# Kernel optimization log

Hardware: AMD Instinct MI355X
Metric: run time of the kernel (lower is better)

Reference implementation:

```python
import jax, jax.numpy as jnp
import numpy as np

B, C, H, W = 8, 256, 128, 128
K = 3  # conv kernel size, padding=1 -> SAME


def conv3x3(x, w, b):
    # x: [B,C,H,W], w: [O,I,K,K], b: [O]
    y = jax.lax.conv_general_dilated(
        x, w, window_strides=(1, 1), padding='SAME',
        dimension_numbers=('NCHW', 'OIHW', 'NCHW'))
    return y + b[None, :, None, None]


def setup_inputs() -> dict:
    key = jax.random.key(0)
    ks = jax.random.split(key, 7)
    fan_in = C * K * K
    s = 1.0 / np.sqrt(fan_in)
    x = jax.random.normal(ks[0], (B, C, H, W), dtype=jnp.float32)
    Wq = jax.random.uniform(ks[1], (C, C, K, K), jnp.float32, -s, s)
    bq = jax.random.uniform(ks[2], (C,), jnp.float32, -s, s)
    Wk = jax.random.uniform(ks[3], (C, C, K, K), jnp.float32, -s, s)
    bk = jax.random.uniform(ks[4], (C,), jnp.float32, -s, s)
    Wv = jax.random.uniform(ks[5], (C, C, K, K), jnp.float32, -s, s)
    bv = jax.random.uniform(ks[6], (C,), jnp.float32, -s, s)
    return {'x': x, 'Wq': Wq, 'bq': bq, 'Wk': Wk, 'bk': bk, 'Wv': Wv, 'bv': bv}


def reference(x, Wq, bq, Wk, bk, Wv, bv):
    b_, c_, h_, w_ = x.shape
    residual = x
    q = jax.nn.relu(conv3x3(x, Wq, bq))  # [B,C,H,W]
    k = jax.nn.relu(conv3x3(x, Wk, bk))  # [B,C,H,W]
    v = conv3x3(x, Wv, bv)               # [B,C,H,W]
    # per-(batch,channel) spatial matmul: [H,W] @ [H,W] -> [H,W] (requires H==W)
    attn = jnp.einsum('bcij,bcjk->bcik', q, k)
    # softmax over the flattened H*W positions jointly per (b,c)
    attn = jax.nn.softmax(attn.reshape(b_, c_, h_ * w_), axis=-1).reshape(b_, c_, h_, w_)
    y = jnp.einsum('bcij,bcjk->bcik', attn, v)
    return y + residual
```

## Files before the change

### kernel.cpp

```cpp
#include <hip/hip_runtime.h>

#define BB 8
#define CC 256
#define HH 128
#define WW 128
#define HW (HH*WW)

typedef float f32x4 __attribute__((ext_vector_type(4)));
typedef short s16x8 __attribute__((ext_vector_type(8)));

__device__ inline unsigned short f2bf(float f) {
  union { float f; unsigned int u; } un;
  un.f = f;
  unsigned int u = un.u;
  return (unsigned short)((u + 0x7fffu + ((u >> 16) & 1u)) >> 16);
}

__global__ __launch_bounds__(256) void k_prepass(const float* __restrict__ x,
                                                 unsigned short* __restrict__ xbf) {
  __shared__ float tile[64][68];
  int bh = blockIdx.x;
  int b = bh >> 7, h = bh & 127;
  int w0 = blockIdx.y * 64;
  int c0 = blockIdx.z * 64;
  int t = threadIdx.x;
  {
    int c = t >> 2, wq = (t & 3) << 4;
    const float4* src = reinterpret_cast<const float4*>(
        x + (((size_t)(b * CC + c0 + c) * HH + h) * WW + w0 + wq));
    float4 v0 = src[0], v1 = src[1], v2 = src[2], v3 = src[3];
    *reinterpret_cast<float4*>(&tile[c][wq + 0])  = v0;
    *reinterpret_cast<float4*>(&tile[c][wq + 4])  = v1;
    *reinterpret_cast<float4*>(&tile[c][wq + 8])  = v2;
    *reinterpret_cast<float4*>(&tile[c][wq + 12]) = v3;
  }
  __syncthreads();
  {
    int w = t >> 2, cg = (t & 3) << 4;
    unsigned short tmp[16];
#pragma unroll
    for (int i = 0; i < 16; ++i) tmp[i] = f2bf(tile[cg + i][w]);
    unsigned short* dst = xbf + ((size_t)(b * HH + h) * WW + w0 + w) * CC + c0 + cg;
    *reinterpret_cast<int4*>(dst)     = *reinterpret_cast<int4*>(tmp);
    *reinterpret_cast<int4*>(dst + 8) = *reinterpret_cast<int4*>(tmp + 8);
  }
}

__global__ __launch_bounds__(256) void k_repack(const float* __restrict__ Wq,
                                                const float* __restrict__ Wk,
                                                const float* __restrict__ Wv,
                                                unsigned short* __restrict__ Wp) {
  int idx = blockIdx.x * 256 + threadIdx.x;
  if (idx >= 8 * 9 * 768 * 32) return;
  int ci = idx & 31;
  int tmp = idx >> 5;
  int focs = tmp % 768;
  int tmp2 = tmp / 768;
  int tap = tmp2 % 9;
  int chunk = tmp2 / 9;
  int cv = focs >> 8, oc = focs & 255;
  int cin = chunk * 32 + ci;
  const float* Wsrc = (cv == 0) ? Wq : ((cv == 1) ? Wk : Wv);
  Wp[idx] = f2bf(Wsrc[(size_t)(oc * 256 + cin) * 9 + tap]);
}

#define PADC 40
__global__ __launch_bounds__(256, 2) void k_conv(const unsigned short* __restrict__ xbf,
                                                 const unsigned short* __restrict__ Wp,
                                                 const float* __restrict__ bq,
                                                 const float* __restrict__ bk,
                                                 const float* __restrict__ bv,
                                                 unsigned short* __restrict__ qkv) {
  __shared__ unsigned short xs[4][132][PADC];
  __shared__ float bias_s[128];
  int bid = blockIdx.x;
  int v_ = (bid & 7) * 384 + (bid >> 3);
  int mtile = v_ % 6;
  int bhp = v_ / 6;
  int b = bhp >> 6;
  int h0 = (bhp & 63) * 2;
  int t = threadIdx.x;
  if (t < 128) {
    int focs = mtile * 128 + t;
    int cv = focs >> 8, oc = focs & 255;
    const float* bp = (cv == 0) ? bq : ((cv == 1) ? bk : bv);
    bias_s[t] = bp[oc];
  }
  int lane = t & 63, wave = t >> 6;
  int wm = wave >> 1, wn = wave & 1;
  int l15 = lane & 15, lg = lane >> 4;
  f32x4 acc[4][8] = {};
  for (int chunk = 0; chunk < 8; ++chunk) {
    __syncthreads();
    for (int g = t; g < 2080; g += 256) {
      int oct = g & 3;
      int wc = (g >> 2) % 130;
      int r = (g >> 2) / 130;
      int hin = h0 + r - 1, win = wc - 1;
      int4 val = {0, 0, 0, 0};
      if ((unsigned)hin < 128u && (unsigned)win < 128u) {
        val = *reinterpret_cast<const int4*>(
            xbf + ((size_t)(b * HH + hin) * WW + win) * CC + chunk * 32 + oct * 8);
      }
      *reinterpret_cast<int4*>(&xs[r][wc][oct * 8]) = val;
    }
    __syncthreads();
    const unsigned short* wpc = Wp + (size_t)chunk * (9 * 768 * 32)
                                + (size_t)(mtile * 128 + wm * 64 + l15) * 32 + lg * 8;
#pragma unroll
    for (int tap = 0; tap < 9; ++tap) {
      const int r = tap / 3, s = tap % 3;
      s16x8 afr[4], bfr[8];
      const unsigned short* ap = wpc + tap * (768 * 32);
#pragma unroll
      for (int m = 0; m < 4; ++m)
        afr[m] = *reinterpret_cast<const s16x8*>(ap + m * (16 * 32));
#pragma unroll
      for (int n = 0; n < 8; ++n)
        bfr[n] = *reinterpret_cast<const s16x8*>(&xs[wn + r][n * 16 + l15 + s][lg * 8]);
#pragma unroll
      for (int m = 0; m < 4; ++m)
#pragma unroll
        for (int n = 0; n < 8; ++n)
          acc[m][n] = __builtin_amdgcn_mfma_f32_16x16x32_bf16(afr[m], bfr[n], acc[m][n], 0, 0, 0);
    }
  }
#pragma unroll
  for (int m = 0; m < 4; ++m) {
#pragma unroll
    for (int n = 0; n < 8; ++n) {
      int wcol = n * 16 + l15;
      int h = h0 + wn;
#pragma unroll
      for (int rg = 0; rg < 4; ++rg) {
        int rl = wm * 64 + m * 16 + lg * 4 + rg;
        float vv = acc[m][n][rg] + bias_s[rl];
        int focs = mtile * 128 + rl;
        if (focs < 512) vv = fmaxf(vv, 0.0f);
        int cv = focs >> 8, oc = focs & 255;
        qkv[(size_t)(cv * 2048 + b * 256 + oc) * HW + h * WW + wcol] = f2bf(vv);
      }
    }
  }
}

#define PADA 136
__global__ __launch_bounds__(256) void k_attn(const unsigned short* __restrict__ qkv,
                                              const float* __restrict__ x,
                                              float* __restrict__ out) {
  __shared__ unsigned short al[128][PADA];
  __shared__ unsigned short kt[128][PADA];
  __shared__ unsigned short vt[128][PADA];
  __shared__ float red[8];
  int bc = blockIdx.x;
  const unsigned short* qp = qkv + (size_t)bc * HW;
  const unsigned short* kp = qkv + (size_t)(2048 + bc) * HW;
  const unsigned short* vp = qkv + (size_t)(4096 + bc) * HW;
  int t = threadIdx.x;
  for (int g = t; g < HW; g += 256) {
    int row = g >> 7, col = g & 127;
    kt[col][row] = kp[g];
    vt[col][row] = vp[g];
  }
  __syncthreads();
  int lane = t & 63, wave = t >> 6;
  int wm = wave >> 1, wn = wave & 1;
  int l15 = lane & 15, lg = lane >> 4;
  f32x4 acc[4][4] = {};
#pragma unroll
  for (int kk = 0; kk < 4; ++kk) {
    s16x8 af[4], bfr[4];
#pragma unroll
    for (int m = 0; m < 4; ++m)
      af[m] = *reinterpret_cast<const s16x8*>(qp + (size_t)(wm * 64 + m * 16 + l15) * WW + kk * 32 + lg * 8);
#pragma unroll
    for (int n = 0; n < 4; ++n)
      bfr[n] = *reinterpret_cast<const s16x8*>(&kt[wn * 64 + n * 16 + l15][kk * 32 + lg * 8]);
#pragma unroll
    for (int m = 0; m < 4; ++m)
#pragma unroll
      for (int n = 0; n < 4; ++n)
        acc[m][n] = __builtin_amdgcn_mfma_f32_16x16x32_bf16(af[m], bfr[n], acc[m][n], 0, 0, 0);
  }
  float lm = -3.0e38f;
#pragma unroll
  for (int m = 0; m < 4; ++m)
#pragma unroll
    for (int n = 0; n < 4; ++n)
#pragma unroll
      for (int rg = 0; rg < 4; ++rg)
        lm = fmaxf(lm, acc[m][n][rg]);
  for (int off = 32; off > 0; off >>= 1) lm = fmaxf(lm, __shfl_xor(lm, off));
  if (lane == 0) red[wave] = lm;
  __syncthreads();
  float M = fmaxf(fmaxf(red[0], red[1]), fmaxf(red[2], red[3]));
  float ls = 0.0f;
#pragma unroll
  for (int m = 0; m < 4; ++m)
#pragma unroll
    for (int n = 0; n < 4; ++n)
#pragma unroll
      for (int rg = 0; rg < 4; ++rg)
        ls += __expf(acc[m][n][rg] - M);
  for (int off = 32; off > 0; off >>= 1) ls += __shfl_xor(ls, off);
  if (lane == 0) red[4 + wave] = ls;
  __syncthreads();
  float inv = 1.0f / (red[4] + red[5] + red[6] + red[7]);
#pragma unroll
  for (int m = 0; m < 4; ++m) {
#pragma unroll
    for (int n = 0; n < 4; ++n) {
      int col = wn * 64 + n * 16 + l15;
#pragma unroll
      for (int rg = 0; rg < 4; ++rg) {
        int row = wm * 64 + m * 16 + lg * 4 + rg;
        al[row][col] = f2bf(__expf(acc[m][n][rg] - M) * inv);
      }
    }
  }
  __syncthreads();
  f32x4 o_[4][4] = {};
#pragma unroll
  for (int kk = 0; kk < 4; ++kk) {
    s16x8 af[4], bfr[4];
#pragma unroll
    for (int m = 0; m < 4; ++m)
      af[m] = *reinterpret_cast<const s16x8*>(&al[wm * 64 + m * 16 + l15][kk * 32 + lg * 8]);
#pragma unroll
    for (int n = 0; n < 4; ++n)
      bfr[n] = *reinterpret_cast<const s16x8*>(&vt[wn * 64 + n * 16 + l15][kk * 32 + lg * 8]);
#pragma unroll
    for (int m = 0; m < 4; ++m)
#pragma unroll
      for (int n = 0; n < 4; ++n)
        o_[m][n] = __builtin_amdgcn_mfma_f32_16x16x32_bf16(af[m], bfr[n], o_[m][n], 0, 0, 0);
  }
  const float* xp = x + (size_t)bc * HW;
  float* op = out + (size_t)bc * HW;
#pragma unroll
  for (int m = 0; m < 4; ++m) {
#pragma unroll
    for (int n = 0; n < 4; ++n) {
      int col = wn * 64 + n * 16 + l15;
#pragma unroll
      for (int rg = 0; rg < 4; ++rg) {
        int row = wm * 64 + m * 16 + lg * 4 + rg;
        op[row * WW + col] = o_[m][n][rg] + xp[row * WW + col];
      }
    }
  }
}

extern "C" void kernel_launch(void* const* d_in, const int* in_sizes, int n_in,
                              void* d_out, int out_size, void* d_ws, size_t ws_size,
                              hipStream_t stream) {
  const float* x  = (const float*)d_in[0];
  const float* Wq = (const float*)d_in[1];
  const float* bq = (const float*)d_in[2];
  const float* Wk = (const float*)d_in[3];
  const float* bk = (const float*)d_in[4];
  const float* Wv = (const float*)d_in[5];
  const float* bv = (const float*)d_in[6];
  float* out = (float*)d_out;

  unsigned short* xbf = (unsigned short*)d_ws;
  unsigned short* qkv = xbf + (size_t)33554432;
  unsigned short* Wp  = qkv + (size_t)3 * 33554432;

  dim3 g0(1024, 2, 4);
  k_prepass<<<g0, 256, 0, stream>>>(x, xbf);
  k_repack<<<6912, 256, 0, stream>>>(Wq, Wk, Wv, Wp);
  k_conv<<<3072, 256, 0, stream>>>(xbf, Wp, bq, bk, bv, qkv);
  k_attn<<<2048, 256, 0, stream>>>(qkv, x, out);
}
```

Measured before the change: 583.2 us.

## Double-buffer conv input via async global-to-LDS loads with 32x32 MFMA tiles

The conv kernel now stages each 32-channel input chunk into a double-buffered LDS tile using global_load_lds direct copies, prefetching the next chunk while computing the current one. The padding layout is replaced by an XOR swizzle, and out-of-bounds rows read from a zeroed workspace buffer. Compute switches from 16x16x32 to 32x32x16 bf16 MFMA, reusing each loaded input row across the three vertical taps. The aim is to hide load latency, cut barriers and LDS traffic, at the cost of more LDS per block and more complex indexing.

```diff
diff --git a/kernel.cpp b/kernel.cpp
--- a/kernel.cpp
+++ b/kernel.cpp
@@ -7,6 +7,7 @@
 #define HW (HH*WW)
 
 typedef float f32x4 __attribute__((ext_vector_type(4)));
+typedef float f32x16 __attribute__((ext_vector_type(16)));
 typedef short s16x8 __attribute__((ext_vector_type(8)));
 
 __device__ inline unsigned short f2bf(float f) {
@@ -14,6 +15,12 @@
   un.f = f;
   unsigned int u = un.u;
   return (unsigned short)((u + 0x7fffu + ((u >> 16) & 1u)) >> 16);
+}
+
+__device__ __forceinline__ void gload_lds16(const void* g, void* l) {
+  __builtin_amdgcn_global_load_lds(
+      (const __attribute__((address_space(1))) unsigned int*)g,
+      (__attribute__((address_space(3))) unsigned int*)l, 16, 0, 0);
 }
 
 __global__ __launch_bounds__(256) void k_prepass(const float* __restrict__ x,
@@ -49,7 +56,12 @@
 __global__ __launch_bounds__(256) void k_repack(const float* __restrict__ Wq,
                                                 const float* __restrict__ Wk,
                                                 const float* __restrict__ Wv,
-                                                unsigned short* __restrict__ Wp) {
+                                                unsigned short* __restrict__ Wp,
+                                                unsigned short* __restrict__ zp) {
+  if (blockIdx.x == 0 && threadIdx.x < 64) {
+    int4 z = {0, 0, 0, 0};
+    reinterpret_cast<int4*>(zp)[threadIdx.x] = z;
+  }
   int idx = blockIdx.x * 256 + threadIdx.x;
   if (idx >= 8 * 9 * 768 * 32) return;
   int ci = idx & 31;
@@ -64,14 +76,14 @@
   Wp[idx] = f2bf(Wsrc[(size_t)(oc * 256 + cin) * 9 + tap]);
 }
 
-#define PADC 40
 __global__ __launch_bounds__(256, 2) void k_conv(const unsigned short* __restrict__ xbf,
                                                  const unsigned short* __restrict__ Wp,
+                                                 const unsigned short* __restrict__ zp,
                                                  const float* __restrict__ bq,
                                                  const float* __restrict__ bk,
                                                  const float* __restrict__ bv,
                                                  unsigned short* __restrict__ qkv) {
-  __shared__ unsigned short xs[4][132][PADC];
+  __shared__ unsigned short xs[2][4][132][32];
   __shared__ float bias_s[128];
   int bid = blockIdx.x;
   int v_ = (bid & 7) * 384 + (bid >> 3);
@@ -80,65 +92,110 @@
   int b = bhp >> 6;
   int h0 = (bhp & 63) * 2;
   int t = threadIdx.x;
+  int lane = t & 63, wave = t >> 6;
+  int wm = wave >> 1, wq = wave & 1;
+  int l31 = lane & 31, lg1 = lane >> 5;
+
   if (t < 128) {
     int focs = mtile * 128 + t;
     int cv = focs >> 8, oc = focs & 255;
     const float* bp = (cv == 0) ? bq : ((cv == 1) ? bk : bv);
     bias_s[t] = bp[oc];
   }
-  int lane = t & 63, wave = t >> 6;
-  int wm = wave >> 1, wn = wave & 1;
-  int l15 = lane & 15, lg = lane >> 4;
-  f32x4 acc[4][8] = {};
+  {
+    int cell = t >> 4;
+    int bf_ = cell >> 3, r_ = (cell >> 1) & 3;
+    int wc_ = (cell & 1) ? 129 : 0;
+    *reinterpret_cast<int*>(reinterpret_cast<char*>(&xs[bf_][r_][wc_][0]) + (t & 15) * 4) = 0;
+  }
+
+  int l2 = lane >> 2, l4 = lane & 3;
+  int osw = l4 ^ (((l2 + 1) >> 1) & 3);
+  int rsta = wave;
+  int hin = h0 + rsta - 1;
+  bool inb = ((unsigned)hin < 128u);
+  const unsigned short* srow =
+      xbf + ((size_t)(b * HH + (inb ? hin : 0)) * WW + l2) * CC + osw * 8;
+  const unsigned short* zsrc = zp + lane * 8;
+
+  auto STAGE = [&](int bufn, int chunk) {
+    char* d0 = reinterpret_cast<char*>(&xs[bufn][rsta][1][0]);
+    if (inb) {
+      const unsigned short* s0 = srow + chunk * 32;
+#pragma unroll
+      for (int j = 0; j < 8; ++j)
+        gload_lds16(s0 + j * (16 * CC), d0 + j * 1024);
+    } else {
+#pragma unroll
+      for (int j = 0; j < 8; ++j)
+        gload_lds16(zsrc, d0 + j * 1024);
+    }
+  };
+
+  f32x16 acc[2][2][2] = {};
+  STAGE(0, 0);
+  __syncthreads();
+  int buf = 0;
   for (int chunk = 0; chunk < 8; ++chunk) {
-    __syncthreads();
-    for (int g = t; g < 2080; g += 256) {
-      int oct = g & 3;
-      int wc = (g >> 2) % 130;
-      int r = (g >> 2) / 130;
-      int hin = h0 + r - 1, win = wc - 1;
-      int4 val = {0, 0, 0, 0};
-      if ((unsigned)hin < 128u && (unsigned)win < 128u) {
-        val = *reinterpret_cast<const int4*>(
-            xbf + ((size_t)(b * HH + hin) * WW + win) * CC + chunk * 32 + oct * 8);
+    if (chunk < 7) STAGE(buf ^ 1, chunk + 1);
+    const unsigned short (*xsb)[132][32] = xs[buf];
+    const unsigned short* ap0 = Wp + (size_t)chunk * (9 * 768 * 32)
+        + (size_t)(mtile * 128 + wm * 64 + l31) * 32 + lg1 * 8;
+#pragma unroll
+    for (int ss = 0; ss < 3; ++ss) {
+#pragma unroll
+      for (int kk = 0; kk < 2; ++kk) {
+        s16x8 Bf[4][2];
+#pragma unroll
+        for (int rin = 0; rin < 4; ++rin)
+#pragma unroll
+        for (int nt = 0; nt < 2; ++nt) {
+          int wc = wq * 64 + nt * 32 + l31 + ss;
+          int pslot = (kk * 2 + lg1) ^ ((wc >> 1) & 3);
+          Bf[rin][nt] = *reinterpret_cast<const s16x8*>(
+              reinterpret_cast<const char*>(&xsb[rin][0][0]) + wc * 64 + pslot * 16);
+        }
+        s16x8 Af[3][2];
+#pragma unroll
+        for (int rr = 0; rr < 3; ++rr)
+#pragma unroll
+        for (int mt = 0; mt < 2; ++mt)
+          Af[rr][mt] = *reinterpret_cast<const s16x8*>(
+              ap0 + (rr * 3 + ss) * (768 * 32) + mt * 1024 + kk * 16);
+#pragma unroll
+        for (int rr = 0; rr < 3; ++rr)
+#pragma unroll
+        for (int row = 0; row < 2; ++row)
+#pragma unroll
+        for (int mt = 0; mt < 2; ++mt)
+#pragma unroll
+        for (int nt = 0; nt < 2; ++nt)
+          acc[mt][row][nt] = __builtin_amdgcn_mfma_f32_32x32x16_bf16(
+              Af[rr][mt], Bf[row + rr][nt], acc[mt][row][nt], 0, 0, 0);
       }
-      *reinterpret_cast<int4*>(&xs[r][wc][oct * 8]) = val;
-    }
-    __syncthreads();
-    const unsigned short* wpc = Wp + (size_t)chunk * (9 * 768 * 32)
-                                + (size_t)(mtile * 128 + wm * 64 + l15) * 32 + lg * 8;
-#pragma unroll
-    for (int tap = 0; tap < 9; ++tap) {
-      const int r = tap / 3, s = tap % 3;
-      s16x8 afr[4], bfr[8];
-      const unsigned short* ap = wpc + tap * (768 * 32);
-#pragma unroll
-      for (int m = 0; m < 4; ++m)
-        afr[m] = *reinterpret_cast<const s16x8*>(ap + m * (16 * 32));
-#pragma unroll
-      for (int n = 0; n < 8; ++n)
-        bfr[n] = *reinterpret_cast<const s16x8*>(&xs[wn + r][n * 16 + l15 + s][lg * 8]);
-#pragma unroll
-      for (int m = 0; m < 4; ++m)
-#pragma unroll
-        for (int n = 0; n < 8; ++n)
-          acc[m][n] = __builtin_amdgcn_mfma_f32_16x16x32_bf16(afr[m], bfr[n], acc[m][n], 0, 0, 0);
-    }
-  }
-#pragma unroll
-  for (int m = 0; m < 4; ++m) {
-#pragma unroll
-    for (int n = 0; n < 8; ++n) {
-      int wcol = n * 16 + l15;
-      int h = h0 + wn;
-#pragma unroll
-      for (int rg = 0; rg < 4; ++rg) {
-        int rl = wm * 64 + m * 16 + lg * 4 + rg;
-        float vv = acc[m][n][rg] + bias_s[rl];
-        int focs = mtile * 128 + rl;
-        if (focs < 512) vv = fmaxf(vv, 0.0f);
-        int cv = focs >> 8, oc = focs & 255;
-        qkv[(size_t)(cv * 2048 + b * 256 + oc) * HW + h * WW + wcol] = f2bf(vv);
+    }
+    if (chunk < 7) __syncthreads();
+    buf ^= 1;
+  }
+
+#pragma unroll
+  for (int mt = 0; mt < 2; ++mt) {
+#pragma unroll
+    for (int row = 0; row < 2; ++row) {
+#pragma unroll
+      for (int nt = 0; nt < 2; ++nt) {
+        int wcol = wq * 64 + nt * 32 + l31;
+        int h = h0 + row;
+#pragma unroll
+        for (int reg = 0; reg < 16; ++reg) {
+          int rloc = (reg & 3) + 8 * (reg >> 2) + 4 * lg1;
+          int floc = wm * 64 + mt * 32 + rloc;
+          float vv = acc[mt][row][nt][reg] + bias_s[floc];
+          int focs = mtile * 128 + floc;
+          if (focs < 512) vv = fmaxf(vv, 0.0f);
+          int cv = focs >> 8, oc = focs & 255;
+          qkv[(size_t)(cv * 2048 + b * 256 + oc) * HW + h * WW + wcol] = f2bf(vv);
+        }
       }
     }
   }
@@ -266,10 +323,11 @@
   unsigned short* xbf = (unsigned short*)d_ws;
   unsigned short* qkv = xbf + (size_t)33554432;
   unsigned short* Wp  = qkv + (size_t)3 * 33554432;
+  unsigned short* zp  = Wp + (size_t)(8 * 9 * 768 * 32);
 
   dim3 g0(1024, 2, 4);
   k_prepass<<<g0, 256, 0, stream>>>(x, xbf);
-  k_repack<<<6912, 256, 0, stream>>>(Wq, Wk, Wv, Wp);
-  k_conv<<<3072, 256, 0, stream>>>(xbf, Wp, bq, bk, bv, qkv);
+  k_repack<<<6912, 256, 0, stream>>>(Wq, Wk, Wv, Wp, zp);
+  k_conv<<<3072, 256, 0, stream>>>(xbf, Wp, zp, bq, bk, bv, qkv);
   k_attn<<<2048, 256, 0, stream>>>(qkv, x, out);
 }
```

New measurement: 575.5 us. About the same (-1.3%).

## Rewrite conv to read padded channel-plane input directly with 32x32 MFMA

Applied to the files above, without the earlier changes.

The prepass now writes input as bf16 planes of 8 channels with zero-padded width columns, plus a zeroed row buffer for out-of-range rows. The conv kernel drops its LDS staging and barriers and loads B fragments straight from global memory via row pointers. It switches to 32x32x16 MFMA with smaller 64-output tiles, twice the blocks, and occupancy 3, and adds setprio around the MFMA bursts. This trades LDS reuse for redundant global/L2 reads of input rows.

```diff
diff --git a/kernel.cpp b/kernel.cpp
--- a/kernel.cpp
+++ b/kernel.cpp
@@ -6,7 +6,10 @@
 #define WW 128
 #define HW (HH*WW)
 
+#define PLANE_B (128 * 130 * 16)
+
 typedef float f32x4 __attribute__((ext_vector_type(4)));
+typedef float f32x16 __attribute__((ext_vector_type(16)));
 typedef short s16x8 __attribute__((ext_vector_type(8)));
 
 __device__ inline unsigned short f2bf(float f) {
@@ -17,7 +20,7 @@
 }
 
 __global__ __launch_bounds__(256) void k_prepass(const float* __restrict__ x,
-                                                 unsigned short* __restrict__ xbf) {
+                                                 char* __restrict__ xb2) {
   __shared__ float tile[64][68];
   int bh = blockIdx.x;
   int b = bh >> 7, h = bh & 127;
@@ -35,14 +38,23 @@
     *reinterpret_cast<float4*>(&tile[c][wq + 12]) = v3;
   }
   __syncthreads();
-  {
-    int w = t >> 2, cg = (t & 3) << 4;
-    unsigned short tmp[16];
-#pragma unroll
-    for (int i = 0; i < 16; ++i) tmp[i] = f2bf(tile[cg + i][w]);
-    unsigned short* dst = xbf + ((size_t)(b * HH + h) * WW + w0 + w) * CC + c0 + cg;
-    *reinterpret_cast<int4*>(dst)     = *reinterpret_cast<int4*>(tmp);
-    *reinterpret_cast<int4*>(dst + 8) = *reinterpret_cast<int4*>(tmp + 8);
+  int w = t & 63, cgi = t >> 6;
+#pragma unroll
+  for (int j2 = 0; j2 < 2; ++j2) {
+    int cgl = cgi * 2 + j2;
+    unsigned short tmp[8];
+#pragma unroll
+    for (int i = 0; i < 8; ++i) tmp[i] = f2bf(tile[cgl * 8 + i][w]);
+    size_t off = (size_t)(b * 32 + blockIdx.z * 8 + cgl) * PLANE_B
+               + ((size_t)h * 130 + (w0 + w + 1)) * 16;
+    *reinterpret_cast<int4*>(xb2 + off) = *reinterpret_cast<int4*>(tmp);
+  }
+  if (t < 8) {
+    int4 z = {0, 0, 0, 0};
+    int wp = (blockIdx.y == 0) ? 0 : 129;
+    size_t off = (size_t)(b * 32 + blockIdx.z * 8 + t) * PLANE_B
+               + ((size_t)h * 130 + wp) * 16;
+    *reinterpret_cast<int4*>(xb2 + off) = z;
   }
 }
 
@@ -64,78 +76,93 @@
   Wp[idx] = f2bf(Wsrc[(size_t)(oc * 256 + cin) * 9 + tap]);
 }
 
-#define PADC 40
-__global__ __launch_bounds__(256, 2) void k_conv(const unsigned short* __restrict__ xbf,
+__global__ __launch_bounds__(256, 3) void k_conv(const char* __restrict__ xb2,
                                                  const unsigned short* __restrict__ Wp,
                                                  const float* __restrict__ bq,
                                                  const float* __restrict__ bk,
                                                  const float* __restrict__ bv,
                                                  unsigned short* __restrict__ qkv) {
-  __shared__ unsigned short xs[4][132][PADC];
-  __shared__ float bias_s[128];
+  __shared__ float bias_s[64];
   int bid = blockIdx.x;
-  int v_ = (bid & 7) * 384 + (bid >> 3);
-  int mtile = v_ % 6;
-  int bhp = v_ / 6;
+  int v_ = (bid & 7) * 768 + (bid >> 3);
+  int mtile = v_ % 12;
+  int bhp = v_ / 12;
   int b = bhp >> 6;
   int h0 = (bhp & 63) * 2;
   int t = threadIdx.x;
-  if (t < 128) {
-    int focs = mtile * 128 + t;
+  int lane = t & 63, wave = t >> 6;
+  int wm = wave >> 1, wq = wave & 1;
+  int l31 = lane & 31, lg1 = lane >> 5;
+
+  if (t < 64) {
+    int focs = mtile * 64 + t;
     int cv = focs >> 8, oc = focs & 255;
     const float* bp = (cv == 0) ? bq : ((cv == 1) ? bk : bv);
     bias_s[t] = bp[oc];
   }
-  int lane = t & 63, wave = t >> 6;
-  int wm = wave >> 1, wn = wave & 1;
-  int l15 = lane & 15, lg = lane >> 4;
-  f32x4 acc[4][8] = {};
+  __syncthreads();
+
+  const char* zbase = xb2 + (size_t)256 * PLANE_B;
+  int woff[2];
+#pragma unroll
+  for (int nt = 0; nt < 2; ++nt)
+    woff[nt] = (lg1 * (128 * 130) + (wq * 64 + nt * 32 + l31)) * 16;
+
+  const size_t CH_STRIDE = (size_t)9 * 768 * 32;
+  const unsigned short* apbase = Wp + (size_t)(mtile * 64 + wm * 32 + l31) * 32 + lg1 * 8;
+
+  f32x16 acc[2][2] = {};
+
   for (int chunk = 0; chunk < 8; ++chunk) {
-    __syncthreads();
-    for (int g = t; g < 2080; g += 256) {
-      int oct = g & 3;
-      int wc = (g >> 2) % 130;
-      int r = (g >> 2) / 130;
-      int hin = h0 + r - 1, win = wc - 1;
-      int4 val = {0, 0, 0, 0};
-      if ((unsigned)hin < 128u && (unsigned)win < 128u) {
-        val = *reinterpret_cast<const int4*>(
-            xbf + ((size_t)(b * HH + hin) * WW + win) * CC + chunk * 32 + oct * 8);
-      }
-      *reinterpret_cast<int4*>(&xs[r][wc][oct * 8]) = val;
+    const unsigned short* ap = apbase + chunk * CH_STRIDE;
+#pragma unroll
+    for (int kk = 0; kk < 2; ++kk) {
+      const char* rowb[4];
+#pragma unroll
+      for (int rin = 0; rin < 4; ++rin) {
+        int hin = h0 + rin - 1;
+        rowb[rin] = ((unsigned)hin < 128u)
+            ? xb2 + (size_t)(b * 32 + chunk * 4 + kk * 2) * PLANE_B + (size_t)hin * (130 * 16)
+            : zbase;
+      }
+#pragma unroll
+      for (int ss = 0; ss < 3; ++ss) {
+        s16x8 Bf[4][2];
+#pragma unroll
+        for (int rin = 0; rin < 4; ++rin)
+#pragma unroll
+        for (int nt = 0; nt < 2; ++nt)
+          Bf[rin][nt] = *reinterpret_cast<const s16x8*>(rowb[rin] + woff[nt] + ss * 16);
+        s16x8 Af[3];
+#pragma unroll
+        for (int rr = 0; rr < 3; ++rr)
+          Af[rr] = *reinterpret_cast<const s16x8*>(ap + (rr * 3 + ss) * (768 * 32) + kk * 16);
+        __builtin_amdgcn_s_setprio(1);
+#pragma unroll
+        for (int rr = 0; rr < 3; ++rr)
+#pragma unroll
+        for (int row = 0; row < 2; ++row)
+#pragma unroll
+        for (int nt = 0; nt < 2; ++nt)
+          acc[row][nt] = __builtin_amdgcn_mfma_f32_32x32x16_bf16(
+              Af[rr], Bf[row + rr][nt], acc[row][nt], 0, 0, 0);
+        __builtin_amdgcn_s_setprio(0);
+      }
     }
-    __syncthreads();
-    const unsigned short* wpc = Wp + (size_t)chunk * (9 * 768 * 32)
-                                + (size_t)(mtile * 128 + wm * 64 + l15) * 32 + lg * 8;
-#pragma unroll
-    for (int tap = 0; tap < 9; ++tap) {
-      const int r = tap / 3, s = tap % 3;
-      s16x8 afr[4], bfr[8];
-      const unsigned short* ap = wpc + tap * (768 * 32);
-#pragma unroll
-      for (int m = 0; m < 4; ++m)
-        afr[m] = *reinterpret_cast<const s16x8*>(ap + m * (16 * 32));
-#pragma unroll
-      for (int n = 0; n < 8; ++n)
-        bfr[n] = *reinterpret_cast<const s16x8*>(&xs[wn + r][n * 16 + l15 + s][lg * 8]);
-#pragma unroll
-      for (int m = 0; m < 4; ++m)
-#pragma unroll
-        for (int n = 0; n < 8; ++n)
-          acc[m][n] = __builtin_amdgcn_mfma_f32_16x16x32_bf16(afr[m], bfr[n], acc[m][n], 0, 0, 0);
-    }
-  }
-#pragma unroll
-  for (int m = 0; m < 4; ++m) {
-#pragma unroll
-    for (int n = 0; n < 8; ++n) {
-      int wcol = n * 16 + l15;
-      int h = h0 + wn;
-#pragma unroll
-      for (int rg = 0; rg < 4; ++rg) {
-        int rl = wm * 64 + m * 16 + lg * 4 + rg;
-        float vv = acc[m][n][rg] + bias_s[rl];
-        int focs = mtile * 128 + rl;
+  }
+
+#pragma unroll
+  for (int row = 0; row < 2; ++row) {
+#pragma unroll
+    for (int nt = 0; nt < 2; ++nt) {
+      int wcol = wq * 64 + nt * 32 + l31;
+      int h = h0 + row;
+#pragma unroll
+      for (int reg = 0; reg < 16; ++reg) {
+        int rloc = (reg & 3) + 8 * (reg >> 2) + 4 * lg1;
+        int floc = wm * 32 + rloc;
+        float vv = acc[row][nt][reg] + bias_s[floc];
+        int focs = mtile * 64 + floc;
         if (focs < 512) vv = fmaxf(vv, 0.0f);
         int cv = focs >> 8, oc = focs & 255;
         qkv[(size_t)(cv * 2048 + b * 256 + oc) * HW + h * WW + wcol] = f2bf(vv);
@@ -263,13 +290,16 @@
   const float* bv = (const float*)d_in[6];
   float* out = (float*)d_out;
 
-  unsigned short* xbf = (unsigned short*)d_ws;
-  unsigned short* qkv = xbf + (size_t)33554432;
-  unsigned short* Wp  = qkv + (size_t)3 * 33554432;
-
+  char* xb2 = (char*)d_ws;
+  size_t zoff = (size_t)256 * PLANE_B;
+  unsigned short* qkv = (unsigned short*)(xb2 + zoff + 270336);
+  unsigned short* Wp  = qkv + (size_t)3 * BB * 256 * HW / 6 * 6;
+  Wp = qkv + (size_t)100663296;
+
+  hipMemsetAsync(xb2 + zoff, 0, 270336, stream);
   dim3 g0(1024, 2, 4);
-  k_prepass<<<g0, 256, 0, stream>>>(x, xbf);
+  k_prepass<<<g0, 256, 0, stream>>>(x, xb2);
   k_repack<<<6912, 256, 0, stream>>>(Wq, Wk, Wv, Wp);
-  k_conv<<<3072, 256, 0, stream>>>(xbf, Wp, bq, bk, bv, qkv);
+  k_conv<<<6144, 256, 0, stream>>>(xb2, Wp, bq, bk, bv, qkv);
   k_attn<<<2048, 256, 0, stream>>>(qkv, x, out);
 }
```

Measured after the change: 760.2 us. 30.3% more time.
